# Kernel optimization log

Measured on AMD Instinct MI355X. Metric: run time of the kernel, lower is better.

## Reference

```python
import jax, jax.numpy as jnp
import numpy as np

H, W, HID = 7, 7, 512
IN_DIM = 1024

def _grid_edges(h, w):
    e = []
    for r in range(h):
        for c in range(w):
            n = r * w + c
            if c < w - 1:
                e.append((n, n + 1))
            if r < h - 1:
                e.append((n, n + w))
    return np.asarray(e, dtype=np.int32).T  # [2, 84]

_BASE = _grid_edges(H, W)

def setup_inputs() -> dict:
    key = jax.random.key(0)
    ks = jax.random.split(key, 16)
    B = 1024
    s = 0.02
    return {
        "visual_feat": jax.random.normal(ks[0], (B, 512, H, W), jnp.float32),
        "tactile_feat": jax.random.normal(ks[1], (B, 512, H, W), jnp.float32),
        "proj_W": jax.random.normal(ks[2], (IN_DIM, 2), jnp.float32) * s,
        "proj_b": jnp.zeros((2,), jnp.float32),
        "gc1_rel_W": jax.random.normal(ks[3], (IN_DIM, HID), jnp.float32) * s,
        "gc1_rel_b": jnp.zeros((HID,), jnp.float32),
        "gc1_root_W": jax.random.normal(ks[4], (IN_DIM, HID), jnp.float32) * s,
        "bn1_gamma": jnp.ones((HID,), jnp.float32),
        "bn1_beta": jnp.zeros((HID,), jnp.float32),
        "gc2_rel_W": jax.random.normal(ks[5], (HID, HID), jnp.float32) * s,
        "gc2_rel_b": jnp.zeros((HID,), jnp.float32),
        "gc2_root_W": jax.random.normal(ks[6], (HID, HID), jnp.float32) * s,
        "bn2_gamma": jnp.ones((HID,), jnp.float32),
        "bn2_beta": jnp.zeros((HID,), jnp.float32),
        "dec_W": jax.random.normal(ks[7], (HID + 1, HID), jnp.float32) * s,
        "dec_b": jnp.zeros((HID,), jnp.float32),
    }

def _batched_edges(B):
    off = (np.arange(B, dtype=np.int32) * (H * W))[:, None]
    src = (_BASE[0][None, :] + off).reshape(-1)
    dst = (_BASE[1][None, :] + off).reshape(-1)
    return jnp.asarray(src), jnp.asarray(dst)

def _bn(x, gamma, beta):
    mu = x.mean(0)
    var = x.var(0)  # biased, matches torch BN normalization
    return (x - mu) * jax.lax.rsqrt(var + 1e-5) * gamma + beta

def _graph_conv(x, src, dst, ew, W_rel, b_rel, W_root, N):
    msg = ew[:, None] * x[src]                      # [E, D]
    agg = jax.ops.segment_sum(msg, dst, num_segments=N)
    deg = jax.ops.segment_sum(jnp.ones_like(ew), dst, num_segments=N)
    agg = agg / jnp.maximum(deg, 1.0)[:, None]
    return agg @ W_rel + b_rel + x @ W_root

def reference(visual_feat, tactile_feat, proj_W, proj_b,
              gc1_rel_W, gc1_rel_b, gc1_root_W, bn1_gamma, bn1_beta,
              gc2_rel_W, gc2_rel_b, gc2_root_W, bn2_gamma, bn2_beta,
              dec_W, dec_b):
    B = visual_feat.shape[0]
    N = B * H * W
    # node features: concat channels, NCHW -> N x (2C)
    node = jnp.concatenate([visual_feat, tactile_feat], axis=1)
    node = node.transpose(0, 2, 3, 1).reshape(N, IN_DIM)
    src, dst = _batched_edges(B)
    coords = node @ proj_W + proj_b                 # [N, 2]
    dist = jnp.linalg.norm(coords[src] - coords[dst], axis=1)
    edge_attr = jax.nn.sigmoid(1.0 / (dist + 1e-6))  # [E]
    alpha = jnp.exp(edge_attr)
    alpha = alpha / (alpha.sum() + 1e-8)            # global normalization over all edges
    x = jax.nn.relu(_bn(_graph_conv(node, src, dst, alpha, gc1_rel_W, gc1_rel_b, gc1_root_W, N), bn1_gamma, bn1_beta))
    x = jax.nn.relu(_bn(_graph_conv(x, src, dst, alpha, gc2_rel_W, gc2_rel_b, gc2_root_W, N), bn2_gamma, bn2_beta))
    # scatter_mean of edge_attr over both endpoints
    ids = jnp.concatenate([src, dst])
    vals = jnp.concatenate([edge_attr, edge_attr])
    nw_sum = jax.ops.segment_sum(vals, ids, num_segments=N)
    nw_cnt = jax.ops.segment_sum(jnp.ones_like(vals), ids, num_segments=N)
    node_w = nw_sum / jnp.maximum(nw_cnt, 1.0)      # [N]
    x = jax.nn.relu(jnp.concatenate([x, node_w[:, None]], axis=1) @ dec_W + dec_b)
    return x.reshape(B, H, W, HID).transpose(0, 3, 1, 2)
```

## Files before the change

### kernel.cpp

```cpp
#include <hip/hip_runtime.h>
#include <hip/hip_bf16.h>

typedef float f32x4 __attribute__((ext_vector_type(4)));
typedef short s16x8 __attribute__((ext_vector_type(8)));

#define N_NODES 50176

static __device__ __forceinline__ ushort f2bf(float x) {
    __hip_bfloat16 h = __float2bfloat16(x);
    return *reinterpret_cast<ushort*>(&h);
}
static __device__ __forceinline__ float bf2f(ushort u) {
    __hip_bfloat16 h = *reinterpret_cast<__hip_bfloat16*>(&u);
    return __bfloat162float(h);
}

static __device__ __forceinline__ void gload_lds16(const void* g, void* l) {
    __builtin_amdgcn_global_load_lds((const __attribute__((address_space(1))) void*)g,
                                     (__attribute__((address_space(3))) void*)l, 16, 0, 0);
}

__global__ void k_prep0(const float* W2r, const float* W2t, const float* decW,
                        ushort* Bt2, ushort* Bt3, float* decLast, float* alpha_sum, float* bn_acc) {
    int idx = blockIdx.x * 256 + threadIdx.x;
    if (idx < 512 * 1024) {
        int j = idx >> 10, k = idx & 1023;
        float v = (k < 512) ? W2r[k * 512 + j] : W2t[(k - 512) * 512 + j];
        Bt2[idx] = f2bf(v);
    }
    if (idx < 512 * 512) {
        int j = idx >> 9, k = idx & 511;
        Bt3[idx] = f2bf(decW[k * 512 + j]);
    }
    if (idx < 512) decLast[idx] = decW[512 * 512 + idx];
    if (idx < 2048) bn_acc[idx] = 0.f;
    if (idx == 0) alpha_sum[0] = 0.f;
}

__global__ void k_prep1(const float* W1r, const float* W1t, const float* asum, ushort* Bt1) {
    int idx = blockIdx.x * 256 + threadIdx.x;
    int j = idx >> 11, k = idx & 2047;
    float s = 1.f / (asum[0] + 1e-8f);
    float v = (k < 1024) ? W1r[k * 512 + j] * s : W1t[(k - 1024) * 512 + j];
    Bt1[idx] = f2bf(v);
}

__global__ __launch_bounds__(256) void k_front(const float* __restrict__ vis, const float* __restrict__ tac,
                                               const float* __restrict__ projW, const float* __restrict__ projb,
                                               ushort* __restrict__ xcat1, float* __restrict__ ew_exp,
                                               float* __restrict__ node_w, float* __restrict__ alpha_sum) {
    int b = blockIdx.x, tid = threadIdx.x;
    __shared__ ushort tile[128 * 50];
    __shared__ float pw[2048];
    __shared__ float cx[52], cy[52], ea[84], eex[84], wsum[4];
    __shared__ float wl[49], wt[49];
    for (int p = tid; p < 2048; p += 256) pw[p] = projW[p];
    float a0t = 0.f, a1t = 0.f;
    const int cn = tid >> 2, dl = tid & 3;
    for (int chunk = 0; chunk < 8; ++chunk) {
        __syncthreads();
        const float* src = (chunk < 4 ? vis : tac) + ((size_t)b * 512 + (chunk & 3) * 128) * 49;
        for (int p = tid; p < 128 * 49; p += 256) {
            int d = p / 49, n = p - d * 49;
            tile[d * 50 + n] = f2bf(src[p]);
        }
        __syncthreads();
        for (int p = tid; p < 49 * 64; p += 256) {
            int n = p >> 6, d2 = (p & 63) * 2;
            ushort2 o;
            o.x = tile[d2 * 50 + n];
            o.y = tile[(d2 + 1) * 50 + n];
            *(ushort2*)&xcat1[((size_t)(b * 49 + n)) * 2048 + 1024 + chunk * 128 + d2] = o;
        }
        if (tid < 196) {
#pragma unroll 4
            for (int j = 0; j < 32; ++j) {
                int d = dl + 4 * j;
                float v = bf2f(tile[d * 50 + cn]);
                int gd = chunk * 128 + d;
                a0t += v * pw[2 * gd];
                a1t += v * pw[2 * gd + 1];
            }
        }
    }
    a0t += __shfl_down(a0t, 1); a1t += __shfl_down(a1t, 1);
    a0t += __shfl_down(a0t, 2); a1t += __shfl_down(a1t, 2);
    if (tid < 196 && dl == 0) { cx[cn] = a0t + projb[0]; cy[cn] = a1t + projb[1]; }
    __syncthreads();
    float ex = 0.f;
    if (tid < 84) {
        int s, d2;
        if (tid < 42) { int r = tid / 6, c = tid - r * 6; s = r * 7 + c; d2 = s + 1; }
        else { int t = tid - 42; int r = t / 7, c = t - r * 7; s = r * 7 + c; d2 = s + 7; }
        float dx = cx[s] - cx[d2], dy = cy[s] - cy[d2];
        float dist = sqrtf(dx * dx + dy * dy);
        float attr = 1.f / (1.f + expf(-(1.f / (dist + 1e-6f))));
        ea[tid] = attr;
        ex = expf(attr);
        eex[tid] = ex;
        ew_exp[b * 84 + tid] = ex;
    }
    for (int off = 32; off; off >>= 1) ex += __shfl_down(ex, off);
    if ((tid & 63) == 0) wsum[tid >> 6] = ex;
    __syncthreads();
    if (tid == 0) atomicAdd(alpha_sum, wsum[0] + wsum[1] + wsum[2] + wsum[3]);
    if (tid < 49) {
        int r = tid / 7, c = tid - r * 7;
        float s = 0.f; int cnt = 0;
        if (c > 0) { s += ea[r * 6 + c - 1]; cnt++; }
        if (c < 6) { s += ea[r * 6 + c]; cnt++; }
        if (r > 0) { s += ea[42 + (r - 1) * 7 + c]; cnt++; }
        if (r < 6) { s += ea[42 + r * 7 + c]; cnt++; }
        node_w[b * 49 + tid] = s / (float)cnt;
        int deg = (c > 0) + (r > 0);
        float inv = deg ? 1.f / (float)deg : 0.f;
        wl[tid] = (c > 0) ? eex[r * 6 + c - 1] * inv : 0.f;
        wt[tid] = (r > 0) ? eex[42 + (r - 1) * 7 + c] * inv : 0.f;
    }
    __syncthreads();
    ushort* base = xcat1 + (size_t)b * 49 * 2048;
    for (int idx = tid; idx < 49 * 128; idx += 256) {
        int n = idx >> 7, ch = idx & 127;
        float w1 = wl[n], w2 = wt[n];
        float acc[8];
#pragma unroll
        for (int k = 0; k < 8; ++k) acc[k] = 0.f;
        if (w1 != 0.f) {
            s16x8 u = *(const s16x8*)(base + (size_t)(n - 1) * 2048 + 1024 + ch * 8);
#pragma unroll
            for (int k = 0; k < 8; ++k) acc[k] += w1 * bf2f((ushort)u[k]);
        }
        if (w2 != 0.f) {
            s16x8 u = *(const s16x8*)(base + (size_t)(n - 7) * 2048 + 1024 + ch * 8);
#pragma unroll
            for (int k = 0; k < 8; ++k) acc[k] += w2 * bf2f((ushort)u[k]);
        }
        s16x8 o;
#pragma unroll
        for (int k = 0; k < 8; ++k) o[k] = (short)f2bf(acc[k]);
        *(s16x8*)(base + (size_t)n * 2048 + ch * 8) = o;
    }
}

template <int EPI>
__global__ __launch_bounds__(256, 2)
void k_gemm(const ushort* __restrict__ A, const ushort* __restrict__ Bt, float* __restrict__ C,
            int K,
            const float* __restrict__ bias, float* __restrict__ bn_sum, float* __restrict__ bn_sumsq,
            const float* __restrict__ node_w, const float* __restrict__ decLast,
            const float* __restrict__ decb, float* __restrict__ out) {
    __shared__ __align__(16) ushort As[128 * 32];
    __shared__ __align__(16) ushort Bs[128 * 32];
    const int bid = blockIdx.x;
    const int rowb = ((bid & 7) | ((bid >> 5) << 3));
    const int colb = (bid >> 3) & 3;
    const int row0 = rowb << 7, col0 = colb << 7;
    const int tid = threadIdx.x;
    const int lane = tid & 63, wave = tid >> 6;
    const int wm = (wave & 1) << 6, wn = (wave >> 1) << 6;
    const int quad = lane >> 4, l16 = lane & 15;
    const int K8 = K >> 3;

    const uint4* Ag = (const uint4*)A;
    const uint4* Bg = (const uint4*)Bt;

    const int c0 = wave, c1 = wave + 4;
    const int lrow = lane >> 2, lkc = lane & 3;
    const size_t iA0 = (size_t)(row0 + c0 * 16 + lrow) * K8 + lkc;
    const size_t iA1 = (size_t)(row0 + c1 * 16 + lrow) * K8 + lkc;
    const size_t iB0 = (size_t)(col0 + c0 * 16 + lrow) * K8 + lkc;
    const size_t iB1 = (size_t)(col0 + c1 * 16 + lrow) * K8 + lkc;
    ushort* lA0 = As + c0 * 512;
    ushort* lA1 = As + c1 * 512;
    ushort* lB0 = Bs + c0 * 512;
    ushort* lB1 = Bs + c1 * 512;

    f32x4 acc[4][4];
#pragma unroll
    for (int i = 0; i < 4; ++i)
#pragma unroll
        for (int j = 0; j < 4; ++j) acc[i][j] = (f32x4)0.f;

    const int nk = K >> 5;
    for (int kt = 0; kt < nk; ++kt) {
        const size_t o = (size_t)kt * 4;
        gload_lds16(Ag + iA0 + o, lA0);
        gload_lds16(Ag + iA1 + o, lA1);
        gload_lds16(Bg + iB0 + o, lB0);
        gload_lds16(Bg + iB1 + o, lB1);
        __syncthreads();
        s16x8 af[4], bf[4];
#pragma unroll
        for (int i = 0; i < 4; ++i) af[i] = *(const s16x8*)&As[(wm + i * 16 + l16) * 32 + quad * 8];
#pragma unroll
        for (int j = 0; j < 4; ++j) bf[j] = *(const s16x8*)&Bs[(wn + j * 16 + l16) * 32 + quad * 8];
#pragma unroll
        for (int i = 0; i < 4; ++i)
#pragma unroll
            for (int j = 0; j < 4; ++j)
                acc[i][j] = __builtin_amdgcn_mfma_f32_16x16x32_bf16(af[i], bf[j], acc[i][j], 0, 0, 0);
        __syncthreads();
    }

    if (EPI == 0) {
#pragma unroll
        for (int j = 0; j < 4; ++j) {
            int col = col0 + wn + j * 16 + l16;
            float bcol = bias[col];
            float s = 0.f, s2 = 0.f;
#pragma unroll
            for (int i = 0; i < 4; ++i) {
#pragma unroll
                for (int r = 0; r < 4; ++r) {
                    int m = row0 + wm + i * 16 + quad * 4 + r;
                    float v = acc[i][j][r] + bcol;
                    C[(size_t)m * 512 + col] = v;
                    s += v; s2 += v * v;
                }
            }
            s += __shfl_xor(s, 16); s += __shfl_xor(s, 32);
            s2 += __shfl_xor(s2, 16); s2 += __shfl_xor(s2, 32);
            if (quad == 0) { atomicAdd(&bn_sum[col], s); atomicAdd(&bn_sumsq[col], s2); }
        }
    } else {
#pragma unroll
        for (int i = 0; i < 4; ++i) {
#pragma unroll
            for (int j = 0; j < 4; ++j) {
#pragma unroll
                for (int r = 0; r < 4; ++r) {
                    int m = row0 + wm + i * 16 + quad * 4 + r;
                    int n = col0 + wn + j * 16 + l16;
                    float v = acc[i][j][r];
                    v += node_w[m] * decLast[n] + decb[n];
                    v = fmaxf(v, 0.f);
                    int bb = m / 49, sp = m - bb * 49;
                    out[((size_t)bb * 512 + n) * 49 + sp] = v;
                }
            }
        }
    }
}

__global__ __launch_bounds__(256) void k_bnagg(const float* __restrict__ P, const float* __restrict__ ew,
                                               const float* __restrict__ asum,
                                               const float* __restrict__ bn_sum, const float* __restrict__ bn_sumsq,
                                               const float* __restrict__ gamma, const float* __restrict__ beta,
                                               ushort* __restrict__ xcat) {
    int b = blockIdx.x, tid = threadIdx.x;
    __shared__ ushort xl[49 * 512];
    __shared__ float wl[49], wt[49];
    __shared__ float scl_s[512], shf_s[512];
    const float invN = 1.f / (float)N_NODES;
    for (int d = tid; d < 512; d += 256) {
        float mu = bn_sum[d] * invN;
        float var = bn_sumsq[d] * invN - mu * mu;
        float sc = gamma[d] * rsqrtf(var + 1e-5f);
        scl_s[d] = sc;
        shf_s[d] = beta[d] - mu * sc;
    }
    if (tid < 49) {
        int r = tid / 7, c = tid - r * 7;
        int deg = (c > 0) + (r > 0);
        float sc = deg ? (1.f / (asum[0] + 1e-8f)) / (float)deg : 0.f;
        wl[tid] = (c > 0) ? ew[b * 84 + r * 6 + (c - 1)] * sc : 0.f;
        wt[tid] = (r > 0) ? ew[b * 84 + 42 + (r - 1) * 7 + c] * sc : 0.f;
    }
    __syncthreads();
    int dc = tid & 127;
    int sp0 = tid >> 7;
    float4 scl = ((const float4*)scl_s)[dc];
    float4 shf = ((const float4*)shf_s)[dc];
    for (int sp = sp0; sp < 49; sp += 2) {
        float4 v = ((const float4*)(P + ((size_t)b * 49 + sp) * 512))[dc];
        ushort4 o;
        o.x = f2bf(fmaxf(v.x * scl.x + shf.x, 0.f));
        o.y = f2bf(fmaxf(v.y * scl.y + shf.y, 0.f));
        o.z = f2bf(fmaxf(v.z * scl.z + shf.z, 0.f));
        o.w = f2bf(fmaxf(v.w * scl.w + shf.w, 0.f));
        *(ushort4*)&xl[sp * 512 + dc * 4] = o;
        ((ushort4*)(xcat + ((size_t)b * 49 + sp) * 1024 + 512))[dc] = o;
    }
    __syncthreads();
    for (int sp = sp0; sp < 49; sp += 2) {
        float a0 = 0.f, a1 = 0.f, a2 = 0.f, a3 = 0.f;
        float w1 = wl[sp], w2 = wt[sp];
        if (w1 != 0.f) {
            ushort4 u = *(const ushort4*)&xl[(sp - 1) * 512 + dc * 4];
            a0 += w1 * bf2f(u.x); a1 += w1 * bf2f(u.y); a2 += w1 * bf2f(u.z); a3 += w1 * bf2f(u.w);
        }
        if (w2 != 0.f) {
            ushort4 u = *(const ushort4*)&xl[(sp - 7) * 512 + dc * 4];
            a0 += w2 * bf2f(u.x); a1 += w2 * bf2f(u.y); a2 += w2 * bf2f(u.z); a3 += w2 * bf2f(u.w);
        }
        ushort4 o;
        o.x = f2bf(a0); o.y = f2bf(a1); o.z = f2bf(a2); o.w = f2bf(a3);
        ((ushort4*)(xcat + ((size_t)b * 49 + sp) * 1024))[dc] = o;
    }
}

__global__ __launch_bounds__(256) void k_bnapply(const float* __restrict__ x,
                                                 const float* __restrict__ bn_sum, const float* __restrict__ bn_sumsq,
                                                 const float* __restrict__ gamma, const float* __restrict__ beta,
                                                 ushort* __restrict__ xb) {
    int b = blockIdx.x, tid = threadIdx.x;
    __shared__ float scl_s[512], shf_s[512];
    const float invN = 1.f / (float)N_NODES;
    for (int d = tid; d < 512; d += 256) {
        float mu = bn_sum[d] * invN;
        float var = bn_sumsq[d] * invN - mu * mu;
        float sc = gamma[d] * rsqrtf(var + 1e-5f);
        scl_s[d] = sc;
        shf_s[d] = beta[d] - mu * sc;
    }
    __syncthreads();
    const float4* src = (const float4*)(x + (size_t)b * 49 * 512);
    ushort4* dst = (ushort4*)(xb + (size_t)b * 49 * 512);
    for (int idx = tid; idx < 49 * 128; idx += 256) {
        int dc = idx & 127;
        float4 scl = ((const float4*)scl_s)[dc];
        float4 shf = ((const float4*)shf_s)[dc];
        float4 v = src[idx];
        ushort4 o;
        o.x = f2bf(fmaxf(v.x * scl.x + shf.x, 0.f));
        o.y = f2bf(fmaxf(v.y * scl.y + shf.y, 0.f));
        o.z = f2bf(fmaxf(v.z * scl.z + shf.z, 0.f));
        o.w = f2bf(fmaxf(v.w * scl.w + shf.w, 0.f));
        dst[idx] = o;
    }
}

extern "C" void kernel_launch(void* const* d_in, const int* in_sizes, int n_in,
                              void* d_out, int out_size, void* d_ws, size_t ws_size,
                              hipStream_t stream) {
    const float* vis   = (const float*)d_in[0];
    const float* tac   = (const float*)d_in[1];
    const float* projW = (const float*)d_in[2];
    const float* projb = (const float*)d_in[3];
    const float* W1r   = (const float*)d_in[4];
    const float* b1    = (const float*)d_in[5];
    const float* W1t   = (const float*)d_in[6];
    const float* g1    = (const float*)d_in[7];
    const float* be1   = (const float*)d_in[8];
    const float* W2r   = (const float*)d_in[9];
    const float* b2    = (const float*)d_in[10];
    const float* W2t   = (const float*)d_in[11];
    const float* g2    = (const float*)d_in[12];
    const float* be2   = (const float*)d_in[13];
    const float* decW  = (const float*)d_in[14];
    const float* decb  = (const float*)d_in[15];
    float* out = (float*)d_out;

    char* p = (char*)d_ws;
    ushort* X   = (ushort*)p; p += 205520896;
    float*  P   = (float*)p;  p += 102760448;
    float* ew     = (float*)p; p += 344064;
    float* nw     = (float*)p; p += 200704;
    ushort* Bt1   = (ushort*)p; p += 2097152;
    ushort* Bt2   = (ushort*)p; p += 1048576;
    ushort* Bt3   = (ushort*)p; p += 524288;
    float* decLast = (float*)p; p += 2048;
    float* asum   = (float*)p;  p += 256;
    float* bnacc  = (float*)p;  p += 4 * 512 * 4;
    float* bn1s = bnacc, *bn1q = bnacc + 512, *bn2s = bnacc + 1024, *bn2q = bnacc + 1536;

    ushort* xcat1 = X;
    ushort* xcat2 = X;
    ushort* x3b   = X;

    k_prep0<<<2048, 256, 0, stream>>>(W2r, W2t, decW, Bt2, Bt3, decLast, asum, bnacc);
    k_front<<<1024, 256, 0, stream>>>(vis, tac, projW, projb, xcat1, ew, nw, asum);
    k_prep1<<<4096, 256, 0, stream>>>(W1r, W1t, asum, Bt1);

    k_gemm<0><<<392 * 4, 256, 0, stream>>>(xcat1, Bt1, P, 2048, b1, bn1s, bn1q, nullptr, nullptr, nullptr, nullptr);
    k_bnagg<<<1024, 256, 0, stream>>>(P, ew, asum, bn1s, bn1q, g1, be1, xcat2);

    k_gemm<0><<<392 * 4, 256, 0, stream>>>(xcat2, Bt2, P, 1024, b2, bn2s, bn2q, nullptr, nullptr, nullptr, nullptr);
    k_bnapply<<<1024, 256, 0, stream>>>(P, bn2s, bn2q, g2, be2, x3b);

    k_gemm<1><<<392 * 4, 256, 0, stream>>>(x3b, Bt3, nullptr, 512, nullptr, nullptr, nullptr, nw, decLast, decb, out);
}
```

Baseline: 741.8 us.

## Replace GEMM with 256x256-tile, 8-wave double-buffered pipelined kernel

Replaces the 128x128 single-buffered GEMM (one barrier pair per 32-wide K step) with a 256x256 tile kernel using 8 waves, 128-wide K tiles and double-buffered LDS (128 KB). Global-to-LDS loads for the next tile are issued inside four MFMA phases, with explicit vmcnt waits, barriers, setprio and an XOR swizzle to avoid LDS bank conflicts. The aim is to hide memory latency behind compute and raise data reuse per loaded byte. The cost is that the large LDS footprint limits occupancy to one block per CU and the tiling adds a remap of block IDs; 392 blocks on 256 CUs may leave the second wave of blocks underfilled.

```diff
diff --git a/kernel.cpp b/kernel.cpp
--- a/kernel.cpp
+++ b/kernel.cpp
@@ -142,78 +142,185 @@
     }
 }
 
+
+#define STAGE(GMAT, LDSBASE, ROWBASE, KT, HALF)                                     \
+  {                                                                                 \
+    const char* g0 = (const char*)(GMAT)                                            \
+        + (size_t)((ROWBASE) + (HALF) * 128 + (w << 3) + (l >> 3)) * KB             \
+        + (size_t)((KT) * 128 + ((((l & 7) << 4)) ^ (((l >> 5) & 1) << 5)));        \
+    char* d0 = (LDSBASE) + (HALF) * 16384 + (w << 10);                              \
+    gload_lds16(g0, d0);                                                            \
+    gload_lds16(g0 + (size_t)64 * KB, d0 + 8192);                                   \
+  }
+
+#define PH_SYNC_PRE()                                                               \
+    __builtin_amdgcn_sched_barrier(0);                                              \
+    __builtin_amdgcn_s_barrier();                                                   \
+    asm volatile("s_waitcnt lgkmcnt(0)" ::: "memory");                              \
+    __builtin_amdgcn_sched_barrier(0);                                              \
+    __builtin_amdgcn_s_setprio(1);
+
+#define PH_SYNC_POST(DOWAIT)                                                        \
+    __builtin_amdgcn_s_setprio(0);                                                  \
+    __builtin_amdgcn_sched_barrier(0);                                              \
+    DOWAIT;                                                                         \
+    __builtin_amdgcn_s_barrier();
+
+#define PHASE_A(SA, SB, ISSUE, DOWAIT)                                              \
+  {                                                                                 \
+    _Pragma("unroll")                                                               \
+    for (int mi = 0; mi < 4; ++mi) {                                                \
+      int row = wr * 128 + mi * 16 + l16;                                           \
+      int sw = ((row >> 2) & 1) << 5;                                               \
+      af03[mi][0] = *(const s16x8*)((SA) + row * 128 + ((quad * 16) ^ sw));         \
+      af03[mi][1] = *(const s16x8*)((SA) + row * 128 + ((64 + quad * 16) ^ sw));    \
+    }                                                                               \
+    _Pragma("unroll")                                                               \
+    for (int ni = 0; ni < 2; ++ni) {                                                \
+      int row = wc * 64 + ni * 16 + l16;                                            \
+      int sw = ((row >> 2) & 1) << 5;                                               \
+      bf01[ni][0] = *(const s16x8*)((SB) + row * 128 + ((quad * 16) ^ sw));         \
+      bf01[ni][1] = *(const s16x8*)((SB) + row * 128 + ((64 + quad * 16) ^ sw));    \
+    }                                                                               \
+    ISSUE;                                                                          \
+    PH_SYNC_PRE()                                                                   \
+    _Pragma("unroll")                                                               \
+    for (int mi = 0; mi < 4; ++mi)                                                  \
+      _Pragma("unroll")                                                             \
+      for (int ni = 0; ni < 2; ++ni) {                                              \
+        acc[mi][ni] = __builtin_amdgcn_mfma_f32_16x16x32_bf16(af03[mi][0], bf01[ni][0], acc[mi][ni], 0, 0, 0); \
+        acc[mi][ni] = __builtin_amdgcn_mfma_f32_16x16x32_bf16(af03[mi][1], bf01[ni][1], acc[mi][ni], 0, 0, 0); \
+      }                                                                             \
+    PH_SYNC_POST(DOWAIT)                                                            \
+  }
+
+#define PHASE_B(SA, ISSUE, DOWAIT)                                                  \
+  {                                                                                 \
+    _Pragma("unroll")                                                               \
+    for (int mi = 0; mi < 4; ++mi) {                                                \
+      int row = wr * 128 + 64 + mi * 16 + l16;                                      \
+      int sw = ((row >> 2) & 1) << 5;                                               \
+      af47[mi][0] = *(const s16x8*)((SA) + row * 128 + ((quad * 16) ^ sw));         \
+      af47[mi][1] = *(const s16x8*)((SA) + row * 128 + ((64 + quad * 16) ^ sw));    \
+    }                                                                               \
+    ISSUE;                                                                          \
+    PH_SYNC_PRE()                                                                   \
+    _Pragma("unroll")                                                               \
+    for (int mi = 0; mi < 4; ++mi)                                                  \
+      _Pragma("unroll")                                                             \
+      for (int ni = 0; ni < 2; ++ni) {                                              \
+        acc[4 + mi][ni] = __builtin_amdgcn_mfma_f32_16x16x32_bf16(af47[mi][0], bf01[ni][0], acc[4 + mi][ni], 0, 0, 0); \
+        acc[4 + mi][ni] = __builtin_amdgcn_mfma_f32_16x16x32_bf16(af47[mi][1], bf01[ni][1], acc[4 + mi][ni], 0, 0, 0); \
+      }                                                                             \
+    PH_SYNC_POST(DOWAIT)                                                            \
+  }
+
+#define PHASE_C(SB, ISSUE, DOWAIT)                                                  \
+  {                                                                                 \
+    _Pragma("unroll")                                                               \
+    for (int ni = 0; ni < 2; ++ni) {                                                \
+      int row = wc * 64 + 32 + ni * 16 + l16;                                       \
+      int sw = ((row >> 2) & 1) << 5;                                               \
+      bf23[ni][0] = *(const s16x8*)((SB) + row * 128 + ((quad * 16) ^ sw));         \
+      bf23[ni][1] = *(const s16x8*)((SB) + row * 128 + ((64 + quad * 16) ^ sw));    \
+    }                                                                               \
+    ISSUE;                                                                          \
+    PH_SYNC_PRE()                                                                   \
+    _Pragma("unroll")                                                               \
+    for (int mi = 0; mi < 4; ++mi)                                                  \
+      _Pragma("unroll")                                                             \
+      for (int ni = 0; ni < 2; ++ni) {                                              \
+        acc[mi][2 + ni] = __builtin_amdgcn_mfma_f32_16x16x32_bf16(af03[mi][0], bf23[ni][0], acc[mi][2 + ni], 0, 0, 0); \
+        acc[mi][2 + ni] = __builtin_amdgcn_mfma_f32_16x16x32_bf16(af03[mi][1], bf23[ni][1], acc[mi][2 + ni], 0, 0, 0); \
+      }                                                                             \
+    PH_SYNC_POST(DOWAIT)                                                            \
+  }
+
+#define PHASE_D(ISSUE, DOWAIT)                                                      \
+  {                                                                                 \
+    ISSUE;                                                                          \
+    PH_SYNC_PRE()                                                                   \
+    _Pragma("unroll")                                                               \
+    for (int mi = 0; mi < 4; ++mi)                                                  \
+      _Pragma("unroll")                                                             \
+      for (int ni = 0; ni < 2; ++ni) {                                              \
+        acc[4 + mi][2 + ni] = __builtin_amdgcn_mfma_f32_16x16x32_bf16(af47[mi][0], bf23[ni][0], acc[4 + mi][2 + ni], 0, 0, 0); \
+        acc[4 + mi][2 + ni] = __builtin_amdgcn_mfma_f32_16x16x32_bf16(af47[mi][1], bf23[ni][1], acc[4 + mi][2 + ni], 0, 0, 0); \
+      }                                                                             \
+    PH_SYNC_POST(DOWAIT)                                                            \
+  }
+
+#define VWAIT4 asm volatile("s_waitcnt vmcnt(4)" ::: "memory")
+#define VWAIT0 asm volatile("s_waitcnt vmcnt(0)" ::: "memory")
+#define NOISSUE ((void)0)
+
 template <int EPI>
-__global__ __launch_bounds__(256, 2)
-void k_gemm(const ushort* __restrict__ A, const ushort* __restrict__ Bt, float* __restrict__ C,
-            int K,
-            const float* __restrict__ bias, float* __restrict__ bn_sum, float* __restrict__ bn_sumsq,
-            const float* __restrict__ node_w, const float* __restrict__ decLast,
-            const float* __restrict__ decb, float* __restrict__ out) {
-    __shared__ __align__(16) ushort As[128 * 32];
-    __shared__ __align__(16) ushort Bs[128 * 32];
-    const int bid = blockIdx.x;
-    const int rowb = ((bid & 7) | ((bid >> 5) << 3));
-    const int colb = (bid >> 3) & 3;
-    const int row0 = rowb << 7, col0 = colb << 7;
+__global__ __launch_bounds__(512, 2)
+void k_gemm8(const ushort* __restrict__ A, const ushort* __restrict__ Bt, float* __restrict__ C,
+             int K,
+             const float* __restrict__ bias, float* __restrict__ bn_sum, float* __restrict__ bn_sumsq,
+             const float* __restrict__ node_w, const float* __restrict__ decLast,
+             const float* __restrict__ decb, float* __restrict__ out) {
+    __shared__ __align__(16) char lds[131072];
     const int tid = threadIdx.x;
-    const int lane = tid & 63, wave = tid >> 6;
-    const int wm = (wave & 1) << 6, wn = (wave >> 1) << 6;
-    const int quad = lane >> 4, l16 = lane & 15;
-    const int K8 = K >> 3;
-
-    const uint4* Ag = (const uint4*)A;
-    const uint4* Bg = (const uint4*)Bt;
-
-    const int c0 = wave, c1 = wave + 4;
-    const int lrow = lane >> 2, lkc = lane & 3;
-    const size_t iA0 = (size_t)(row0 + c0 * 16 + lrow) * K8 + lkc;
-    const size_t iA1 = (size_t)(row0 + c1 * 16 + lrow) * K8 + lkc;
-    const size_t iB0 = (size_t)(col0 + c0 * 16 + lrow) * K8 + lkc;
-    const size_t iB1 = (size_t)(col0 + c1 * 16 + lrow) * K8 + lkc;
-    ushort* lA0 = As + c0 * 512;
-    ushort* lA1 = As + c1 * 512;
-    ushort* lB0 = Bs + c0 * 512;
-    ushort* lB1 = Bs + c1 * 512;
-
-    f32x4 acc[4][4];
-#pragma unroll
-    for (int i = 0; i < 4; ++i)
+    const int w = tid >> 6, l = tid & 63;
+    const int wr = w >> 2, wc = w & 3;
+    const int l16 = l & 15, quad = l >> 4;
+
+    const int orig = blockIdx.x;
+    const int wg = (orig & 7) * 49 + (orig >> 3);
+    const int colb = wg & 1, rowb = wg >> 1;
+    const int row0 = rowb << 8, col0 = colb << 8;
+
+    const size_t KB = (size_t)K * 2;
+    char* aS0 = lds;
+    char* aS1 = lds + 32768;
+    char* bS0 = lds + 65536;
+    char* bS1 = lds + 98304;
+
+    f32x4 acc[8][4];
+#pragma unroll
+    for (int i = 0; i < 8; ++i)
 #pragma unroll
         for (int j = 0; j < 4; ++j) acc[i][j] = (f32x4)0.f;
 
-    const int nk = K >> 5;
-    for (int kt = 0; kt < nk; ++kt) {
-        const size_t o = (size_t)kt * 4;
-        gload_lds16(Ag + iA0 + o, lA0);
-        gload_lds16(Ag + iA1 + o, lA1);
-        gload_lds16(Bg + iB0 + o, lB0);
-        gload_lds16(Bg + iB1 + o, lB1);
-        __syncthreads();
-        s16x8 af[4], bf[4];
-#pragma unroll
-        for (int i = 0; i < 4; ++i) af[i] = *(const s16x8*)&As[(wm + i * 16 + l16) * 32 + quad * 8];
-#pragma unroll
-        for (int j = 0; j < 4; ++j) bf[j] = *(const s16x8*)&Bs[(wn + j * 16 + l16) * 32 + quad * 8];
-#pragma unroll
-        for (int i = 0; i < 4; ++i)
-#pragma unroll
-            for (int j = 0; j < 4; ++j)
-                acc[i][j] = __builtin_amdgcn_mfma_f32_16x16x32_bf16(af[i], bf[j], acc[i][j], 0, 0, 0);
-        __syncthreads();
+    s16x8 af03[4][2], af47[4][2], bf01[2][2], bf23[2][2];
+
+    STAGE(A, aS0, row0, 0, 0);
+    STAGE(A, aS0, row0, 0, 1);
+    STAGE(Bt, bS0, col0, 0, 0);
+    STAGE(Bt, bS0, col0, 0, 1);
+    STAGE(A, aS1, row0, 1, 0);
+    STAGE(A, aS1, row0, 1, 1);
+    VWAIT4;
+    __builtin_amdgcn_s_barrier();
+
+    const int T = K >> 7;
+    for (int t = 0; t < T; ++t) {
+        const int k1 = 2 * t + 1, k2 = 2 * t + 2, k3 = 2 * t + 3;
+        const bool pf = (t + 1 < T);
+        PHASE_A(aS0, bS0, STAGE(Bt, bS1, col0, k1, 0), NOISSUE);
+        PHASE_B(aS0,      STAGE(Bt, bS1, col0, k1, 1), NOISSUE);
+        PHASE_C(bS0,      if (pf) STAGE(A, aS0, row0, k2, 0), NOISSUE);
+        PHASE_D(          if (pf) STAGE(A, aS0, row0, k2, 1), if (pf) { VWAIT4; } else { VWAIT0; });
+        PHASE_A(aS1, bS1, if (pf) STAGE(Bt, bS0, col0, k2, 0), NOISSUE);
+        PHASE_B(aS1,      if (pf) STAGE(Bt, bS0, col0, k2, 1), NOISSUE);
+        PHASE_C(bS1,      if (pf) STAGE(A, aS1, row0, k3, 0), NOISSUE);
+        PHASE_D(          if (pf) STAGE(A, aS1, row0, k3, 1), VWAIT4);
     }
 
     if (EPI == 0) {
 #pragma unroll
-        for (int j = 0; j < 4; ++j) {
-            int col = col0 + wn + j * 16 + l16;
+        for (int ni = 0; ni < 4; ++ni) {
+            int col = col0 + wc * 64 + ni * 16 + l16;
             float bcol = bias[col];
             float s = 0.f, s2 = 0.f;
 #pragma unroll
-            for (int i = 0; i < 4; ++i) {
+            for (int mi = 0; mi < 8; ++mi) {
 #pragma unroll
                 for (int r = 0; r < 4; ++r) {
-                    int m = row0 + wm + i * 16 + quad * 4 + r;
-                    float v = acc[i][j][r] + bcol;
+                    int m = row0 + wr * 128 + mi * 16 + quad * 4 + r;
+                    float v = acc[mi][ni][r] + bcol;
                     C[(size_t)m * 512 + col] = v;
                     s += v; s2 += v * v;
                 }
@@ -224,14 +331,14 @@
         }
     } else {
 #pragma unroll
-        for (int i = 0; i < 4; ++i) {
-#pragma unroll
-            for (int j = 0; j < 4; ++j) {
+        for (int mi = 0; mi < 8; ++mi) {
+#pragma unroll
+            for (int ni = 0; ni < 4; ++ni) {
 #pragma unroll
                 for (int r = 0; r < 4; ++r) {
-                    int m = row0 + wm + i * 16 + quad * 4 + r;
-                    int n = col0 + wn + j * 16 + l16;
-                    float v = acc[i][j][r];
+                    int m = row0 + wr * 128 + mi * 16 + quad * 4 + r;
+                    int n = col0 + wc * 64 + ni * 16 + l16;
+                    float v = acc[mi][ni][r];
                     v += node_w[m] * decLast[n] + decb[n];
                     v = fmaxf(v, 0.f);
                     int bb = m / 49, sp = m - bb * 49;
@@ -372,11 +479,11 @@
     k_front<<<1024, 256, 0, stream>>>(vis, tac, projW, projb, xcat1, ew, nw, asum);
     k_prep1<<<4096, 256, 0, stream>>>(W1r, W1t, asum, Bt1);
 
-    k_gemm<0><<<392 * 4, 256, 0, stream>>>(xcat1, Bt1, P, 2048, b1, bn1s, bn1q, nullptr, nullptr, nullptr, nullptr);
+    k_gemm8<0><<<392, 512, 0, stream>>>(xcat1, Bt1, P, 2048, b1, bn1s, bn1q, nullptr, nullptr, nullptr, nullptr);
     k_bnagg<<<1024, 256, 0, stream>>>(P, ew, asum, bn1s, bn1q, g1, be1, xcat2);
 
-    k_gemm<0><<<392 * 4, 256, 0, stream>>>(xcat2, Bt2, P, 1024, b2, bn2s, bn2q, nullptr, nullptr, nullptr, nullptr);
+    k_gemm8<0><<<392, 512, 0, stream>>>(xcat2, Bt2, P, 1024, b2, bn2s, bn2q, nullptr, nullptr, nullptr, nullptr);
     k_bnapply<<<1024, 256, 0, stream>>>(P, bn2s, bn2q, g2, be2, x3b);
 
-    k_gemm<1><<<392 * 4, 256, 0, stream>>>(x3b, Bt3, nullptr, 512, nullptr, nullptr, nullptr, nw, decLast, decb, out);
-}
+    k_gemm8<1><<<392, 512, 0, stream>>>(x3b, Bt3, nullptr, 512, nullptr, nullptr, nullptr, nw, decLast, decb, out);
+}
```

Measured after the change: 761.2 us. 2.6% more time.
